# Kernel tuning notes

Measured on AMD Instinct MI355X. Metric: run time of the kernel, lower is better.

The kernel has to match this reference:

```python
import jax, jax.numpy as jnp
import numpy as np

EPS = 1e-6
SIGMA = 0.1  # temperature for pseudo-LBS blend weights


def _quat_rotate(q, v):
    # q: [..., 4] (w, x, y, z) unit quaternions, v: [..., 3]
    qw, qv = q[..., :1], q[..., 1:]
    t = 2.0 * jnp.cross(qv, v)
    return v + qw * t + jnp.cross(qv, t)


def _pairwise_sqdist(a, b):
    # a: [n, d], b: [m, d] -> [n, m]
    return (jnp.sum(a * a, -1, keepdims=True)
            + jnp.sum(b * b, -1)[None, :]
            - 2.0 * (a @ b.T))


def setup_inputs() -> dict:
    N, K, F, V, J, P, M, H = 300000, 80, 64, 6890, 24, 64, 64, 128
    key = jax.random.key(0)
    ks = jax.random.split(key, 16)
    s = lambda i, shape: jax.random.normal(ks[i], shape, dtype=jnp.float32) * 0.05
    return {
        "xyz": jax.random.normal(ks[0], (N, 3), dtype=jnp.float32),
        "feature": jax.random.normal(ks[1], (N, F), dtype=jnp.float32),
        "centers": jax.random.normal(ks[2], (K, F), dtype=jnp.float32),
        "smpl_verts": jax.random.normal(ks[3], (V, 3), dtype=jnp.float32),
        "skinning_weights": jax.random.uniform(ks[4], (V, J), dtype=jnp.float32),
        "body_pose_feature": jax.random.normal(ks[5], (J, P), dtype=jnp.float32),
        "w_body": s(6, (P + F, M)),
        "b_body": jnp.zeros((M,), jnp.float32),
        "w_pos1": s(7, (3 + M, H)),
        "b_pos1": jnp.zeros((H,), jnp.float32),
        "w_pos2": s(8, (H, M)),
        "b_pos2": jnp.zeros((M,), jnp.float32),
        "w_rot": s(9, (M, 4)),
        "b_rot": jnp.zeros((4,), jnp.float32),
        "w_trans": s(10, (M, 3)),
        "b_trans": jnp.zeros((3,), jnp.float32),
    }


def reference(xyz, feature, centers, smpl_verts, skinning_weights,
              body_pose_feature, w_body, b_body, w_pos1, b_pos1,
              w_pos2, b_pos2, w_rot, b_rot, w_trans, b_trans):
    # ---- soft k-means: soft assignment of N points to K garment joints ----
    a = jax.nn.softmax(-_pairwise_sqdist(feature, centers), axis=-1)  # [N, K]
    cnt = a.sum(axis=0) + EPS                                          # [K]
    # weighted segment-reduce: c_assign^T @ xyz, diag(1/count) normalize
    joint_xyz = (a.T @ xyz) / cnt[:, None]      # [K, 3]
    joint_feat = (a.T @ feature) / cnt[:, None]  # [K, F] (cluster centers)

    # ---- KNN (k=1) skin-weight lookup against SMPL canonical verts ----
    idx = jnp.argmin(_pairwise_sqdist(joint_xyz, smpl_verts), axis=-1)  # [K]
    pts_W = skinning_weights[idx]                                        # [K, J]

    # ---- garment pose decoder ----
    body_feat = pts_W @ body_pose_feature                 # [K, P]
    g = jnp.concatenate([body_feat, joint_feat], axis=-1)  # [K, P+F]
    g = jax.nn.gelu(g @ w_body + b_body)                   # [K, M]
    lo, hi = smpl_verts.min(0), smpl_verts.max(0)
    xn = 2.0 * (joint_xyz - lo) / (hi - lo + EPS) - 1.0    # aabb sym-normalize
    h = jax.nn.relu(jnp.concatenate([xn, g], -1) @ w_pos1 + b_pos1)
    g2 = h @ w_pos2 + b_pos2                               # [K, M]
    q = g2 @ w_rot + b_rot
    q = q / (jnp.linalg.norm(q, axis=-1, keepdims=True) + EPS)  # [K, 4]
    t = g2 @ w_trans + b_trans                                   # [K, 3]

    # ---- pseudo-LBS: blend per-joint transforms back to N points ----
    w = jax.nn.softmax(-_pairwise_sqdist(xyz, joint_xyz) / SIGMA, axis=-1)  # [N, K]
    qb = w @ q
    qb = qb / (jnp.linalg.norm(qb, axis=-1, keepdims=True) + EPS)  # [N, 4]
    deformed_xyz = _quat_rotate(qb, xyz) + w @ t                    # [N, 3]
    return deformed_xyz
```

## Files before the change

### kernel.cpp

```cpp
#include <hip/hip_runtime.h>
#include <math.h>

#define N_PTS 300000
#define NJ 80
#define FDIM 64
#define VN 6890
#define NROUND 4688
#define GRID_A 256
#define TOTW 1024
#define SLOT_B 17408

typedef __attribute__((ext_vector_type(8))) short short8;
typedef __attribute__((ext_vector_type(4))) float f32x4;

union Frag { uint32_t u[4]; short8 v; };

__device__ __forceinline__ uint32_t packhi(float a, float b) {
  return (__float_as_uint(a) >> 16) | (__float_as_uint(b) & 0xFFFF0000u);
}
__device__ __forceinline__ uint32_t packlo(float a, float b) {
  float la = a - __uint_as_float(__float_as_uint(a) & 0xFFFF0000u);
  float lb = b - __uint_as_float(__float_as_uint(b) & 0xFFFF0000u);
  return packhi(la, lb);
}

#define DPPF(x, ctrl) __uint_as_float((uint32_t)__builtin_amdgcn_update_dpp( \
    0, (int)__float_as_uint(x), (ctrl), 0xF, 0xF, true))

__device__ __forceinline__ void gl16(const float* g, const void* l) {
  __builtin_amdgcn_global_load_lds(
      (const __attribute__((address_space(1))) void*)g,
      (__attribute__((address_space(3))) void*)l, 16, 0, 0);
}
__device__ __forceinline__ void gl4(const float* g, const void* l) {
  __builtin_amdgcn_global_load_lds(
      (const __attribute__((address_space(1))) void*)g,
      (__attribute__((address_space(3))) void*)l, 4, 0, 0);
}

__global__ __launch_bounds__(256, 1) void kA(
    const float* __restrict__ xyz, const float* __restrict__ feature,
    const float* __restrict__ centers, float* __restrict__ jacc,
    float* __restrict__ part)
{
  __shared__ __align__(16) unsigned char ring[4][2][SLOT_B];
  __shared__ ushort sChi[NJ][72];
  __shared__ ushort sClo[NJ][72];

  const int tid = threadIdx.x;
  const int w = tid >> 6;
  const int l = tid & 63;
  const int i = l & 15;
  const int g = l >> 4;
  const int gw = blockIdx.x * 4 + w;

  auto STAGE = [&](int st, int rs) {
    const float* fb = feature + (size_t)rs * 4096;
    unsigned char* base = &ring[w][st][0];
    const int maxp = min(63, N_PTS - 1 - rs * 64);
#pragma unroll
    for (int k = 0; k < 16; ++k) {
      const int lu = k * 64 + l;
      int ptl = lu >> 4;
      ptl = ptl <= maxp ? ptl : maxp;
      const int gu = ptl * 16 + ((lu & 15) ^ (ptl & 7));
      gl16(fb + gu * 4, base + k * 1024);
    }
    const float* xb = xyz + (size_t)rs * 192;
    const int maxf = 3 * maxp + 2;
#pragma unroll
    for (int k = 0; k < 3; ++k) {
      int fi = k * 64 + l;
      fi = fi <= maxf ? fi : maxf;
      gl4(xb + fi, base + 16384 + k * 256);
    }
  };

  STAGE(0, gw);

  for (int idx = tid; idx < NJ * FDIM; idx += 256) {
    float f = centers[idx];
    sChi[idx >> 6][idx & 63] = (ushort)(__float_as_uint(f) >> 16);
    float lo = f - __uint_as_float(__float_as_uint(f) & 0xFFFF0000u);
    sClo[idx >> 6][idx & 63] = (ushort)(__float_as_uint(lo) >> 16);
  }
  float cn[5];
#pragma unroll
  for (int nt = 0; nt < 5; ++nt) {
    float s = 0.f;
    const float* cp = centers + (size_t)(i + 16 * nt) * FDIM + 8 * g;
#pragma unroll
    for (int e = 0; e < 8; ++e) {
      float a0 = cp[e], a1 = cp[32 + e];
      s += a0 * a0 + a1 * a1;
    }
    s += __shfl_xor(s, 16);
    s += __shfl_xor(s, 32);
    cn[nt] = s;
  }
  __syncthreads();

  f32x4 acc2[5][5];
#pragma unroll
  for (int a = 0; a < 5; ++a)
#pragma unroll
    for (int b = 0; b < 5; ++b) acc2[a][b] = (f32x4){0.f, 0.f, 0.f, 0.f};

  int s2 = 0;
  for (int r = gw; r < NROUND; r += TOTW) {
    {
      int rn = r + TOTW; if (rn > NROUND - 1) rn = NROUND - 1;
      STAGE(s2 ^ 1, rn);
    }
    asm volatile("s_waitcnt vmcnt(19)" ::: "memory");
    __builtin_amdgcn_sched_barrier(0);

    const float* F = (const float*)&ring[w][s2][0];
    const float* X = (const float*)&ring[w][s2][16384];
    const int pbase = r * 64;

    Frag pA[2][5];
#pragma unroll
    for (int cp = 0; cp < 2; ++cp) {
      f32x4 acc1[2][5];
#pragma unroll
      for (int cc = 0; cc < 2; ++cc)
#pragma unroll
        for (int nt = 0; nt < 5; ++nt) acc1[cc][nt] = (f32x4){0.f, 0.f, 0.f, 0.f};

#pragma unroll
      for (int ks = 0; ks < 2; ++ks) {
        Frag ah[2], al[2];
#pragma unroll
        for (int cc = 0; cc < 2; ++cc) {
          const int ptl = 32 * cp + 16 * cc + i;
          const int m = ptl & 7;
          const int j = 8 * ks + 2 * g;
          float4 va = *(const float4*)(F + ptl * 64 + ((j ^ m) << 2));
          float4 vb = *(const float4*)(F + ptl * 64 + (((j + 1) ^ m) << 2));
          ah[cc].u[0] = packhi(va.x, va.y); ah[cc].u[1] = packhi(va.z, va.w);
          ah[cc].u[2] = packhi(vb.x, vb.y); ah[cc].u[3] = packhi(vb.z, vb.w);
          al[cc].u[0] = packlo(va.x, va.y); al[cc].u[1] = packlo(va.z, va.w);
          al[cc].u[2] = packlo(vb.x, vb.y); al[cc].u[3] = packlo(vb.z, vb.w);
        }
#pragma unroll
        for (int nt = 0; nt < 5; ++nt) {
          Frag bh, bl;
          *(uint4*)bh.u = *(const uint4*)&sChi[i + 16 * nt][32 * ks + 8 * g];
          *(uint4*)bl.u = *(const uint4*)&sClo[i + 16 * nt][32 * ks + 8 * g];
#pragma unroll
          for (int cc = 0; cc < 2; ++cc) {
            acc1[cc][nt] = __builtin_amdgcn_mfma_f32_16x16x32_bf16(ah[cc].v, bh.v, acc1[cc][nt], 0, 0, 0);
            acc1[cc][nt] = __builtin_amdgcn_mfma_f32_16x16x32_bf16(al[cc].v, bh.v, acc1[cc][nt], 0, 0, 0);
            acc1[cc][nt] = __builtin_amdgcn_mfma_f32_16x16x32_bf16(ah[cc].v, bl.v, acc1[cc][nt], 0, 0, 0);
          }
        }
      }

#pragma unroll
      for (int cc = 0; cc < 2; ++cc) {
        f32x4 e5[5];
#pragma unroll
        for (int nt = 0; nt < 5; ++nt)
#pragma unroll
          for (int rr = 0; rr < 4; ++rr) e5[nt][rr] = 2.f * acc1[cc][nt][rr] - cn[nt];
        float rs[4];
#pragma unroll
        for (int rr = 0; rr < 4; ++rr) {
          float mm = e5[0][rr];
#pragma unroll
          for (int nt = 1; nt < 5; ++nt) mm = fmaxf(mm, e5[nt][rr]);
          mm = fmaxf(mm, DPPF(mm, 0xB1));
          mm = fmaxf(mm, DPPF(mm, 0x4E));
          mm = fmaxf(mm, DPPF(mm, 0x141));
          mm = fmaxf(mm, DPPF(mm, 0x140));
          float ss = 0.f;
#pragma unroll
          for (int nt = 0; nt < 5; ++nt) {
            float e = __expf(e5[nt][rr] - mm);
            e5[nt][rr] = e;
            ss += e;
          }
          ss += DPPF(ss, 0xB1);
          ss += DPPF(ss, 0x4E);
          ss += DPPF(ss, 0x141);
          ss += DPPF(ss, 0x140);
          rs[rr] = __builtin_amdgcn_rcpf(ss);
        }
        const int pt0 = pbase + 32 * cp + 16 * cc + 4 * g;
#pragma unroll
        for (int nt = 0; nt < 5; ++nt) {
          float p0 = (pt0 + 0 < N_PTS) ? e5[nt][0] * rs[0] : 0.f;
          float p1 = (pt0 + 1 < N_PTS) ? e5[nt][1] * rs[1] : 0.f;
          float p2 = (pt0 + 2 < N_PTS) ? e5[nt][2] * rs[2] : 0.f;
          float p3 = (pt0 + 3 < N_PTS) ? e5[nt][3] * rs[3] : 0.f;
          pA[cp][nt].u[2 * cc + 0] = packhi(p0, p1);
          pA[cp][nt].u[2 * cc + 1] = packhi(p2, p3);
        }
      }
    }

#pragma unroll
    for (int ct = 0; ct < 5; ++ct) {
#pragma unroll
      for (int hf = 0; hf < 2; ++hf) {
        Frag B;
        float x[8];
        if (ct < 4) {
          const int d = 16 * ct + i, jd = d >> 2, db = d & 3;
#pragma unroll
          for (int n = 0; n < 8; ++n) {
            const int pb = (n < 4) ? (4 * g + n) : (16 + 4 * g + (n - 4));
            const int ptl = 32 * hf + pb;
            x[n] = F[ptl * 64 + ((jd ^ (ptl & 7)) << 2) + db];
          }
        } else {
#pragma unroll
          for (int n = 0; n < 8; ++n) {
            const int pb = (n < 4) ? (4 * g + n) : (16 + 4 * g + (n - 4));
            const int ptl = 32 * hf + pb;
            x[n] = (i < 3) ? X[ptl * 3 + i] : (i == 3 ? 1.f : 0.f);
          }
        }
        B.u[0] = packhi(x[0], x[1]); B.u[1] = packhi(x[2], x[3]);
        B.u[2] = packhi(x[4], x[5]); B.u[3] = packhi(x[6], x[7]);
#pragma unroll
        for (int nt = 0; nt < 5; ++nt)
          acc2[nt][ct] = __builtin_amdgcn_mfma_f32_16x16x32_bf16(pA[hf][nt].v, B.v, acc2[nt][ct], 0, 0, 0);
      }
    }

    s2 ^= 1;
  }

  asm volatile("s_waitcnt vmcnt(0)" ::: "memory");
  __syncthreads();
  float* sJ = (float*)&ring[0][0][0];
  for (int idx = tid; idx < 5440; idx += 256) sJ[idx] = 0.f;
  __syncthreads();
#pragma unroll
  for (int ww = 0; ww < 4; ++ww) {
    if (w == ww) {
#pragma unroll
      for (int nt = 0; nt < 5; ++nt)
#pragma unroll
        for (int ct = 0; ct < 5; ++ct) {
          if (ct < 4 || i < 4) {
            const int col = 16 * ct + i;
#pragma unroll
            for (int rr = 0; rr < 4; ++rr)
              sJ[(16 * nt + 4 * g + rr) * 68 + col] += acc2[nt][ct][rr];
          }
        }
    }
    __syncthreads();
  }
  if (part) {
    for (int idx = tid; idx < 5440; idx += 256)
      part[(size_t)blockIdx.x * 5440 + idx] = sJ[idx];
  } else {
    for (int idx = tid; idx < 5440; idx += 256)
      atomicAdd(&jacc[idx], sJ[idx]);
  }
}

__global__ __launch_bounds__(256) void kB(
    const float* __restrict__ jacc, const float* __restrict__ part,
    const float* __restrict__ smpl,
    const float* __restrict__ sw, const float* __restrict__ bpf,
    const float* __restrict__ w_body, const float* __restrict__ b_body,
    const float* __restrict__ w_pos1, const float* __restrict__ b_pos1,
    const float* __restrict__ w_pos2, const float* __restrict__ b_pos2,
    const float* __restrict__ w_rot,  const float* __restrict__ b_rot,
    const float* __restrict__ w_trans,const float* __restrict__ b_trans,
    float* __restrict__ jpack, float* __restrict__ qpack,
    float* __restrict__ tpack)
{
  const int k = blockIdx.x;
  const int tid = threadIdx.x;
  __shared__ float red[3][68];
  __shared__ float sh68[68];
  __shared__ float gin[128];
  __shared__ float in2[67];
  __shared__ float h2[128];
  __shared__ float g2[64];
  __shared__ float q7[8];

  if (part) {
    if (tid < 204) {
      const int c = tid % 68, bg = tid / 68;
      const int b0 = bg * 85, b1 = (bg == 2) ? GRID_A : b0 + 85;
      const float* pk = part + k * 68 + c;
      float s = 0.f;
#pragma unroll 4
      for (int b = b0; b < b1; ++b) s += pk[(size_t)b * 5440];
      red[bg][c] = s;
    }
    __syncthreads();
    if (tid < 68) sh68[tid] = red[0][tid] + red[1][tid] + red[2][tid];
  } else {
    if (tid < 68) sh68[tid] = jacc[k * 68 + tid];
  }
  __syncthreads();

  const float cnt = sh68[67] + 1e-6f;
  const float jx = sh68[64] / cnt;
  const float jy = sh68[65] / cnt;
  const float jz = sh68[66] / cnt;

  if (tid < 64) {
    const int l = tid;
    gin[64 + l] = sh68[l] / cnt;

    float lo0 = 1e30f, lo1 = 1e30f, lo2 = 1e30f;
    float hi0 = -1e30f, hi1 = -1e30f, hi2 = -1e30f;
    float best = 1e30f; int bi = 0;
    for (int v = l; v < VN; v += 64) {
      float x = smpl[v*3], y = smpl[v*3+1], z = smpl[v*3+2];
      lo0 = fminf(lo0, x); hi0 = fmaxf(hi0, x);
      lo1 = fminf(lo1, y); hi1 = fmaxf(hi1, y);
      lo2 = fminf(lo2, z); hi2 = fmaxf(hi2, z);
      float dx = x - jx, dy = y - jy, dz = z - jz;
      float d = dx*dx + dy*dy + dz*dz;
      if (d < best) { best = d; bi = v; }
    }
#pragma unroll
    for (int m = 1; m < 64; m <<= 1) {
      lo0 = fminf(lo0, __shfl_xor(lo0, m));
      lo1 = fminf(lo1, __shfl_xor(lo1, m));
      lo2 = fminf(lo2, __shfl_xor(lo2, m));
      hi0 = fmaxf(hi0, __shfl_xor(hi0, m));
      hi1 = fmaxf(hi1, __shfl_xor(hi1, m));
      hi2 = fmaxf(hi2, __shfl_xor(hi2, m));
      float d2 = __shfl_xor(best, m); int i2 = __shfl_xor(bi, m);
      if (d2 < best || (d2 == best && i2 < bi)) { best = d2; bi = i2; }
    }

    {
      float s = 0.f;
      for (int j = 0; j < 24; ++j) s += sw[bi*24 + j] * bpf[j*64 + l];
      gin[l] = s;
    }
    if (l < 3) {
      float lo = (l == 0) ? lo0 : (l == 1) ? lo1 : lo2;
      float hi = (l == 0) ? hi0 : (l == 1) ? hi1 : hi2;
      float jc = (l == 0) ? jx : (l == 1) ? jy : jz;
      in2[l] = 2.f * (jc - lo) / (hi - lo + 1e-6f) - 1.f;
    }
  }
  __syncthreads();

  if (tid < 64) {
    const int l = tid;
    float s = b_body[l];
    for (int t = 0; t < 128; ++t) s += gin[t] * w_body[t*64 + l];
    float u = 0.7978845608028654f * (s + 0.044715f * s * s * s);
    float e = __expf(2.f * u);
    float th = 1.f - 2.f / (e + 1.f);
    in2[3 + l] = 0.5f * s * (1.f + th);
  }
  __syncthreads();

  if (tid < 64) {
    const int l = tid;
#pragma unroll
    for (int half = 0; half < 2; ++half) {
      const int m = l + 64*half;
      float s = b_pos1[m];
      for (int t = 0; t < 67; ++t) s += in2[t] * w_pos1[t*128 + m];
      h2[m] = fmaxf(s, 0.f);
    }
  }
  __syncthreads();

  if (tid < 64) {
    const int l = tid;
    float s = b_pos2[l];
    for (int t = 0; t < 128; ++t) s += h2[t] * w_pos2[t*64 + l];
    g2[l] = s;
  }
  __syncthreads();

  if (tid < 4) {
    float s = b_rot[tid];
    for (int t = 0; t < 64; ++t) s += g2[t] * w_rot[t*4 + tid];
    q7[tid] = s;
  } else if (tid < 7) {
    const int j = tid - 4;
    float s = b_trans[j];
    for (int t = 0; t < 64; ++t) s += g2[t] * w_trans[t*3 + j];
    q7[tid] = s;
  }
  __syncthreads();
  if (tid == 0) {
    float q0 = q7[0], q1 = q7[1], q2 = q7[2], q3 = q7[3];
    float rn = 1.f / (sqrtf(q0*q0 + q1*q1 + q2*q2 + q3*q3) + 1e-6f);
    *(float4*)&qpack[k*4] = make_float4(q0*rn, q1*rn, q2*rn, q3*rn);
    *(float4*)&tpack[k*4] = make_float4(q7[4], q7[5], q7[6], 0.f);
    *(float4*)&jpack[k*4] = make_float4(jx, jy, jz, jx*jx + jy*jy + jz*jz);
  }
}

__global__ __launch_bounds__(256) void kC(
    const float* __restrict__ xyz, const float* __restrict__ jpack,
    const float* __restrict__ qpack, const float* __restrict__ tpack,
    float* __restrict__ out)
{
  __shared__ float4 sj[NJ], sq[NJ], st[NJ];
  __shared__ float sxy[768];
  const int tid = threadIdx.x;
  const int pbase = blockIdx.x * 256;
  const int nval = min(256, N_PTS - pbase);
  const int cnt3 = nval * 3;

  if (tid < 80)        sj[tid]       = ((const float4*)jpack)[tid];
  else if (tid < 160)  sq[tid - 80]  = ((const float4*)qpack)[tid - 80];
  else if (tid < 240)  st[tid - 160] = ((const float4*)tpack)[tid - 160];
  for (int t = tid; t < cnt3; t += 256) sxy[t] = xyz[(size_t)pbase * 3 + t];
  __syncthreads();

  const bool valid = tid < nval;
  float x0 = 0.f, x1 = 0.f, x2 = 0.f;
  if (valid) { x0 = sxy[tid*3]; x1 = sxy[tid*3+1]; x2 = sxy[tid*3+2]; }
  __syncthreads();

  float lv[NJ];
  float m = -1e30f;
#pragma unroll
  for (int k = 0; k < NJ; ++k) {
    float4 j = sj[k];
    lv[k] = (2.f*(x0*j.x + x1*j.y + x2*j.z) - j.w) * 10.0f;
    m = fmaxf(m, lv[k]);
  }
  float s = 0.f;
  float qb0=0,qb1=0,qb2=0,qb3=0, tb0=0,tb1=0,tb2=0;
#pragma unroll
  for (int k = 0; k < NJ; ++k) {
    float e = __expf(lv[k] - m);
    s += e;
    float4 q = sq[k];
    float4 t = st[k];
    qb0 += e*q.x; qb1 += e*q.y; qb2 += e*q.z; qb3 += e*q.w;
    tb0 += e*t.x; tb1 += e*t.y; tb2 += e*t.z;
  }
  float rs = 1.f / s;
  qb0*=rs; qb1*=rs; qb2*=rs; qb3*=rs; tb0*=rs; tb1*=rs; tb2*=rs;
  float nrm = sqrtf(qb0*qb0+qb1*qb1+qb2*qb2+qb3*qb3) + 1e-6f;
  float rn = 1.f / nrm;
  float qw = qb0*rn, qx = qb1*rn, qy = qb2*rn, qz = qb3*rn;
  float t2x = 2.f*(qy*x2 - qz*x1);
  float t2y = 2.f*(qz*x0 - qx*x2);
  float t2z = 2.f*(qx*x1 - qy*x0);
  float cx = qy*t2z - qz*t2y;
  float cy = qz*t2x - qx*t2z;
  float cz = qx*t2y - qy*t2x;
  float r0 = x0 + qw*t2x + cx + tb0;
  float r1 = x1 + qw*t2y + cy + tb1;
  float r2 = x2 + qw*t2z + cz + tb2;

  if (valid) { sxy[tid*3] = r0; sxy[tid*3+1] = r1; sxy[tid*3+2] = r2; }
  __syncthreads();
  for (int t = tid; t < cnt3; t += 256) out[(size_t)pbase * 3 + t] = sxy[t];
}

extern "C" void kernel_launch(void* const* d_in, const int* in_sizes, int n_in,
                              void* d_out, int out_size, void* d_ws, size_t ws_size,
                              hipStream_t stream) {
  const float* xyz     = (const float*)d_in[0];
  const float* feature = (const float*)d_in[1];
  const float* centers = (const float*)d_in[2];
  const float* smpl    = (const float*)d_in[3];
  const float* sw      = (const float*)d_in[4];
  const float* bpf     = (const float*)d_in[5];
  const float* w_body  = (const float*)d_in[6];
  const float* b_body  = (const float*)d_in[7];
  const float* w_pos1  = (const float*)d_in[8];
  const float* b_pos1  = (const float*)d_in[9];
  const float* w_pos2  = (const float*)d_in[10];
  const float* b_pos2  = (const float*)d_in[11];
  const float* w_rot   = (const float*)d_in[12];
  const float* b_rot   = (const float*)d_in[13];
  const float* w_trans = (const float*)d_in[14];
  const float* b_trans = (const float*)d_in[15];
  float* out = (float*)d_out;

  float* ws    = (float*)d_ws;
  float* jacc  = ws;
  float* jpack = ws + 5440;
  float* qpack = ws + 5760;
  float* tpack = ws + 6080;
  float* part  = ws + 6400;

  const size_t need = (size_t)6400 + (size_t)GRID_A * 5440;
  const bool use_part = (ws_size / 4) >= need;
  float* part_arg = use_part ? part : nullptr;

  if (!use_part) hipMemsetAsync(jacc, 0, 5440 * sizeof(float), stream);
  kA<<<dim3(GRID_A), dim3(256), 0, stream>>>(xyz, feature, centers, jacc, part_arg);
  kB<<<dim3(NJ), dim3(256), 0, stream>>>(jacc, part_arg, smpl, sw, bpf,
                                         w_body, b_body, w_pos1, b_pos1,
                                         w_pos2, b_pos2, w_rot, b_rot,
                                         w_trans, b_trans, jpack, qpack, tpack);
  kC<<<dim3((N_PTS + 255) / 256), dim3(256), 0, stream>>>(xyz, jpack, qpack, tpack, out);
}
```

Measured before the change: 137.1 us.

## Pre-pack features into MFMA B-operand tiles and halve per-round tile size

Adds a pre-pass kernel that converts feature and xyz into bf16 tiles already in the MFMA B-operand layout, so the main kernel's second GEMM loads B fragments directly instead of gathering and packing scalars from LDS. Each round now covers 32 points instead of 64, which shrinks the LDS ring and register footprint. It also folds log2(e) into the centers so the softmax can use exp2 without a per-element multiply. In exchange it adds an extra kernel launch and roughly 48 MB of extra global traffic for the packed copy, and it depends on the workspace being large enough.

```diff
diff --git a/kernel.cpp b/kernel.cpp
--- a/kernel.cpp
+++ b/kernel.cpp
@@ -5,10 +5,11 @@
 #define NJ 80
 #define FDIM 64
 #define VN 6890
-#define NROUND 4688
+#define NROUND 9375
 #define GRID_A 256
 #define TOTW 1024
-#define SLOT_B 17408
+#define SLOT_B 13312
+#define NTILE 9375
 
 typedef __attribute__((ext_vector_type(8))) short short8;
 typedef __attribute__((ext_vector_type(4))) float f32x4;
@@ -23,6 +24,10 @@
   float lb = b - __uint_as_float(__float_as_uint(b) & 0xFFFF0000u);
   return packhi(la, lb);
 }
+__device__ __forceinline__ uint32_t rne16(float f) {
+  uint32_t u = __float_as_uint(f);
+  return (u + 0x7FFFu + ((u >> 16) & 1u)) >> 16;
+}
 
 #define DPPF(x, ctrl) __uint_as_float((uint32_t)__builtin_amdgcn_update_dpp( \
     0, (int)__float_as_uint(x), (ctrl), 0xF, 0xF, true))
@@ -38,10 +43,67 @@
       (__attribute__((address_space(3))) void*)l, 4, 0, 0);
 }
 
+__global__ __launch_bounds__(256) void kF(
+    const float* __restrict__ xyz, const float* __restrict__ feature,
+    unsigned char* __restrict__ dtb)
+{
+  __shared__ float sF[64][68];
+  __shared__ float sx[192];
+  const int tid = threadIdx.x;
+  const int pbase = blockIdx.x * 64;
+  const int t0 = blockIdx.x * 2;
+
+#pragma unroll
+  for (int q = 0; q < 4; ++q) {
+    int idx = tid + 256 * q;
+    int pt = idx >> 4;
+    int dc = (idx & 15) << 2;
+    int gpt = pbase + pt; if (gpt >= N_PTS) gpt = N_PTS - 1;
+    float4 v = *(const float4*)(feature + (size_t)gpt * FDIM + dc);
+    *(float4*)&sF[pt][dc] = v;
+  }
+  if (tid < 192) {
+    int fi = pbase * 3 + tid;
+    if (fi >= N_PTS * 3) fi = N_PTS * 3 - 1;
+    sx[tid] = xyz[fi];
+  }
+  __syncthreads();
+
+  for (int u = tid; u < 640; u += 256) {
+    const int tile2 = u / 320;
+    const int unit  = u % 320;
+    const int gtile = t0 + tile2;
+    if (gtile >= NTILE) continue;
+    const int d  = unit >> 2;
+    const int gp = unit & 3;
+    const int g  = gp ^ ((d >> 2) & 3);
+    uint32_t wk[4];
+#pragma unroll
+    for (int h = 0; h < 4; ++h) {
+      float v0 = 0.f, v1 = 0.f;
+#pragma unroll
+      for (int z = 0; z < 2; ++z) {
+        const int e = 2 * h + z;
+        const int pl = (e < 4) ? (4 * g + e) : (16 + 4 * g + (e - 4));
+        const int p = 32 * tile2 + pl;
+        float v;
+        if (d < 64)       v = sF[p][d];
+        else if (d < 67)  v = sx[p * 3 + (d - 64)];
+        else if (d == 67) v = 1.f;
+        else              v = 0.f;
+        if (z == 0) v0 = v; else v1 = v;
+      }
+      wk[h] = rne16(v0) | (rne16(v1) << 16);
+    }
+    *(uint4*)(dtb + (size_t)gtile * 5120 + (size_t)unit * 16) = *(uint4*)wk;
+  }
+}
+
+template<int MODE>
 __global__ __launch_bounds__(256, 1) void kA(
     const float* __restrict__ xyz, const float* __restrict__ feature,
-    const float* __restrict__ centers, float* __restrict__ jacc,
-    float* __restrict__ part)
+    const float* __restrict__ centers, const unsigned char* __restrict__ dtb,
+    float* __restrict__ jacc, float* __restrict__ part)
 {
   __shared__ __align__(16) unsigned char ring[4][2][SLOT_B];
   __shared__ ushort sChi[NJ][72];
@@ -55,33 +117,38 @@
   const int gw = blockIdx.x * 4 + w;
 
   auto STAGE = [&](int st, int rs) {
-    const float* fb = feature + (size_t)rs * 4096;
+    const float* fb = feature + (size_t)rs * 2048;
     unsigned char* base = &ring[w][st][0];
-    const int maxp = min(63, N_PTS - 1 - rs * 64);
-#pragma unroll
-    for (int k = 0; k < 16; ++k) {
+#pragma unroll
+    for (int k = 0; k < 8; ++k) {
       const int lu = k * 64 + l;
-      int ptl = lu >> 4;
-      ptl = ptl <= maxp ? ptl : maxp;
+      const int ptl = lu >> 4;
       const int gu = ptl * 16 + ((lu & 15) ^ (ptl & 7));
       gl16(fb + gu * 4, base + k * 1024);
     }
-    const float* xb = xyz + (size_t)rs * 192;
-    const int maxf = 3 * maxp + 2;
-#pragma unroll
-    for (int k = 0; k < 3; ++k) {
-      int fi = k * 64 + l;
-      fi = fi <= maxf ? fi : maxf;
-      gl4(xb + fi, base + 16384 + k * 256);
+    if (MODE == 1) {
+      const unsigned char* db = dtb + (size_t)rs * 5120;
+#pragma unroll
+      for (int k = 0; k < 5; ++k)
+        gl16((const float*)(db + (size_t)k * 1024 + (size_t)l * 16),
+             base + 8192 + k * 1024);
+    } else {
+      const float* xb = xyz + (size_t)rs * 96;
+#pragma unroll
+      for (int k = 0; k < 2; ++k) {
+        int fi = k * 64 + l; if (fi > 95) fi = 95;
+        gl4(xb + fi, base + 8192 + k * 256);
+      }
     }
   };
 
   STAGE(0, gw);
 
   for (int idx = tid; idx < NJ * FDIM; idx += 256) {
-    float f = centers[idx];
-    sChi[idx >> 6][idx & 63] = (ushort)(__float_as_uint(f) >> 16);
-    float lo = f - __uint_as_float(__float_as_uint(f) & 0xFFFF0000u);
+    float cp = centers[idx] * 2.8853900817779268f;
+    uint32_t u = __float_as_uint(cp);
+    sChi[idx >> 6][idx & 63] = (ushort)(u >> 16);
+    float lo = cp - __uint_as_float(u & 0xFFFF0000u);
     sClo[idx >> 6][idx & 63] = (ushort)(__float_as_uint(lo) >> 16);
   }
   float cn[5];
@@ -96,7 +163,7 @@
     }
     s += __shfl_xor(s, 16);
     s += __shfl_xor(s, 32);
-    cn[nt] = s;
+    cn[nt] = s * 1.4426950408889634f;
   }
   __syncthreads();
 
@@ -112,122 +179,116 @@
       int rn = r + TOTW; if (rn > NROUND - 1) rn = NROUND - 1;
       STAGE(s2 ^ 1, rn);
     }
-    asm volatile("s_waitcnt vmcnt(19)" ::: "memory");
+    if constexpr (MODE == 1) asm volatile("s_waitcnt vmcnt(13)" ::: "memory");
+    else                     asm volatile("s_waitcnt vmcnt(10)" ::: "memory");
     __builtin_amdgcn_sched_barrier(0);
 
     const float* F = (const float*)&ring[w][s2][0];
-    const float* X = (const float*)&ring[w][s2][16384];
-    const int pbase = r * 64;
-
-    Frag pA[2][5];
-#pragma unroll
-    for (int cp = 0; cp < 2; ++cp) {
-      f32x4 acc1[2][5];
-#pragma unroll
-      for (int cc = 0; cc < 2; ++cc)
-#pragma unroll
-        for (int nt = 0; nt < 5; ++nt) acc1[cc][nt] = (f32x4){0.f, 0.f, 0.f, 0.f};
-
-#pragma unroll
-      for (int ks = 0; ks < 2; ++ks) {
-        Frag ah[2], al[2];
-#pragma unroll
-        for (int cc = 0; cc < 2; ++cc) {
-          const int ptl = 32 * cp + 16 * cc + i;
-          const int m = ptl & 7;
-          const int j = 8 * ks + 2 * g;
-          float4 va = *(const float4*)(F + ptl * 64 + ((j ^ m) << 2));
-          float4 vb = *(const float4*)(F + ptl * 64 + (((j + 1) ^ m) << 2));
-          ah[cc].u[0] = packhi(va.x, va.y); ah[cc].u[1] = packhi(va.z, va.w);
-          ah[cc].u[2] = packhi(vb.x, vb.y); ah[cc].u[3] = packhi(vb.z, vb.w);
-          al[cc].u[0] = packlo(va.x, va.y); al[cc].u[1] = packlo(va.z, va.w);
-          al[cc].u[2] = packlo(vb.x, vb.y); al[cc].u[3] = packlo(vb.z, vb.w);
+    const unsigned char* Fd = &ring[w][s2][8192];
+    const float* X = (const float*)&ring[w][s2][8192];
+
+    f32x4 acc1[2][5];
+#pragma unroll
+    for (int c = 0; c < 2; ++c)
+#pragma unroll
+      for (int nt = 0; nt < 5; ++nt) acc1[c][nt] = (f32x4){0.f, 0.f, 0.f, 0.f};
+
+#pragma unroll
+    for (int ks = 0; ks < 2; ++ks) {
+      Frag ah[2], al[2];
+#pragma unroll
+      for (int c = 0; c < 2; ++c) {
+        const int ptl = 16 * c + i;
+        const int m = ptl & 7;
+        const int j = 8 * ks + 2 * g;
+        float4 va = *(const float4*)(F + ptl * 64 + ((j ^ m) << 2));
+        float4 vb = *(const float4*)(F + ptl * 64 + (((j + 1) ^ m) << 2));
+        ah[c].u[0] = packhi(va.x, va.y); ah[c].u[1] = packhi(va.z, va.w);
+        ah[c].u[2] = packhi(vb.x, vb.y); ah[c].u[3] = packhi(vb.z, vb.w);
+        al[c].u[0] = packlo(va.x, va.y); al[c].u[1] = packlo(va.z, va.w);
+        al[c].u[2] = packlo(vb.x, vb.y); al[c].u[3] = packlo(vb.z, vb.w);
+      }
+#pragma unroll
+      for (int nt = 0; nt < 5; ++nt) {
+        Frag bh, bl;
+        *(uint4*)bh.u = *(const uint4*)&sChi[i + 16 * nt][32 * ks + 8 * g];
+        *(uint4*)bl.u = *(const uint4*)&sClo[i + 16 * nt][32 * ks + 8 * g];
+#pragma unroll
+        for (int c = 0; c < 2; ++c) {
+          acc1[c][nt] = __builtin_amdgcn_mfma_f32_16x16x32_bf16(ah[c].v, bh.v, acc1[c][nt], 0, 0, 0);
+          acc1[c][nt] = __builtin_amdgcn_mfma_f32_16x16x32_bf16(al[c].v, bh.v, acc1[c][nt], 0, 0, 0);
+          acc1[c][nt] = __builtin_amdgcn_mfma_f32_16x16x32_bf16(ah[c].v, bl.v, acc1[c][nt], 0, 0, 0);
         }
+      }
+    }
+
+    Frag pA[5];
+#pragma unroll
+    for (int c = 0; c < 2; ++c) {
+      f32x4 e5[5];
+#pragma unroll
+      for (int nt = 0; nt < 5; ++nt)
+#pragma unroll
+        for (int rr = 0; rr < 4; ++rr) e5[nt][rr] = acc1[c][nt][rr] - cn[nt];
+      float rs[4];
+#pragma unroll
+      for (int rr = 0; rr < 4; ++rr) {
+        float mm = e5[0][rr];
+#pragma unroll
+        for (int nt = 1; nt < 5; ++nt) mm = fmaxf(mm, e5[nt][rr]);
+        mm = fmaxf(mm, DPPF(mm, 0xB1));
+        mm = fmaxf(mm, DPPF(mm, 0x4E));
+        mm = fmaxf(mm, DPPF(mm, 0x141));
+        mm = fmaxf(mm, DPPF(mm, 0x140));
+        float ss = 0.f;
 #pragma unroll
         for (int nt = 0; nt < 5; ++nt) {
-          Frag bh, bl;
-          *(uint4*)bh.u = *(const uint4*)&sChi[i + 16 * nt][32 * ks + 8 * g];
-          *(uint4*)bl.u = *(const uint4*)&sClo[i + 16 * nt][32 * ks + 8 * g];
-#pragma unroll
-          for (int cc = 0; cc < 2; ++cc) {
-            acc1[cc][nt] = __builtin_amdgcn_mfma_f32_16x16x32_bf16(ah[cc].v, bh.v, acc1[cc][nt], 0, 0, 0);
-            acc1[cc][nt] = __builtin_amdgcn_mfma_f32_16x16x32_bf16(al[cc].v, bh.v, acc1[cc][nt], 0, 0, 0);
-            acc1[cc][nt] = __builtin_amdgcn_mfma_f32_16x16x32_bf16(ah[cc].v, bl.v, acc1[cc][nt], 0, 0, 0);
-          }
+          float e = exp2f(e5[nt][rr] - mm);
+          e5[nt][rr] = e;
+          ss += e;
         }
-      }
-
-#pragma unroll
-      for (int cc = 0; cc < 2; ++cc) {
-        f32x4 e5[5];
-#pragma unroll
-        for (int nt = 0; nt < 5; ++nt)
-#pragma unroll
-          for (int rr = 0; rr < 4; ++rr) e5[nt][rr] = 2.f * acc1[cc][nt][rr] - cn[nt];
-        float rs[4];
-#pragma unroll
-        for (int rr = 0; rr < 4; ++rr) {
-          float mm = e5[0][rr];
-#pragma unroll
-          for (int nt = 1; nt < 5; ++nt) mm = fmaxf(mm, e5[nt][rr]);
-          mm = fmaxf(mm, DPPF(mm, 0xB1));
-          mm = fmaxf(mm, DPPF(mm, 0x4E));
-          mm = fmaxf(mm, DPPF(mm, 0x141));
-          mm = fmaxf(mm, DPPF(mm, 0x140));
-          float ss = 0.f;
-#pragma unroll
-          for (int nt = 0; nt < 5; ++nt) {
-            float e = __expf(e5[nt][rr] - mm);
-            e5[nt][rr] = e;
-            ss += e;
-          }
-          ss += DPPF(ss, 0xB1);
-          ss += DPPF(ss, 0x4E);
-          ss += DPPF(ss, 0x141);
-          ss += DPPF(ss, 0x140);
-          rs[rr] = __builtin_amdgcn_rcpf(ss);
-        }
-        const int pt0 = pbase + 32 * cp + 16 * cc + 4 * g;
-#pragma unroll
-        for (int nt = 0; nt < 5; ++nt) {
-          float p0 = (pt0 + 0 < N_PTS) ? e5[nt][0] * rs[0] : 0.f;
-          float p1 = (pt0 + 1 < N_PTS) ? e5[nt][1] * rs[1] : 0.f;
-          float p2 = (pt0 + 2 < N_PTS) ? e5[nt][2] * rs[2] : 0.f;
-          float p3 = (pt0 + 3 < N_PTS) ? e5[nt][3] * rs[3] : 0.f;
-          pA[cp][nt].u[2 * cc + 0] = packhi(p0, p1);
-          pA[cp][nt].u[2 * cc + 1] = packhi(p2, p3);
-        }
+        ss += DPPF(ss, 0xB1);
+        ss += DPPF(ss, 0x4E);
+        ss += DPPF(ss, 0x141);
+        ss += DPPF(ss, 0x140);
+        rs[rr] = __builtin_amdgcn_rcpf(ss);
+      }
+#pragma unroll
+      for (int nt = 0; nt < 5; ++nt) {
+        pA[nt].u[2 * c + 0] = packhi(e5[nt][0] * rs[0], e5[nt][1] * rs[1]);
+        pA[nt].u[2 * c + 1] = packhi(e5[nt][2] * rs[2], e5[nt][3] * rs[3]);
       }
     }
 
 #pragma unroll
     for (int ct = 0; ct < 5; ++ct) {
-#pragma unroll
-      for (int hf = 0; hf < 2; ++hf) {
-        Frag B;
+      Frag B;
+      if constexpr (MODE == 1) {
+        const int d = 16 * ct + i;
+        const int unit = d * 4 + (g ^ ((i >> 2) & 3));
+        *(uint4*)B.u = *(const uint4*)(Fd + unit * 16);
+      } else {
         float x[8];
         if (ct < 4) {
           const int d = 16 * ct + i, jd = d >> 2, db = d & 3;
 #pragma unroll
           for (int n = 0; n < 8; ++n) {
-            const int pb = (n < 4) ? (4 * g + n) : (16 + 4 * g + (n - 4));
-            const int ptl = 32 * hf + pb;
+            const int ptl = (n < 4) ? (4 * g + n) : (16 + 4 * g + (n - 4));
             x[n] = F[ptl * 64 + ((jd ^ (ptl & 7)) << 2) + db];
           }
         } else {
 #pragma unroll
           for (int n = 0; n < 8; ++n) {
-            const int pb = (n < 4) ? (4 * g + n) : (16 + 4 * g + (n - 4));
-            const int ptl = 32 * hf + pb;
+            const int ptl = (n < 4) ? (4 * g + n) : (16 + 4 * g + (n - 4));
             x[n] = (i < 3) ? X[ptl * 3 + i] : (i == 3 ? 1.f : 0.f);
           }
         }
         B.u[0] = packhi(x[0], x[1]); B.u[1] = packhi(x[2], x[3]);
         B.u[2] = packhi(x[4], x[5]); B.u[3] = packhi(x[6], x[7]);
-#pragma unroll
-        for (int nt = 0; nt < 5; ++nt)
-          acc2[nt][ct] = __builtin_amdgcn_mfma_f32_16x16x32_bf16(pA[hf][nt].v, B.v, acc2[nt][ct], 0, 0, 0);
-      }
+      }
+#pragma unroll
+      for (int nt = 0; nt < 5; ++nt)
+        acc2[nt][ct] = __builtin_amdgcn_mfma_f32_16x16x32_bf16(pA[nt].v, B.v, acc2[nt][ct], 0, 0, 0);
     }
 
     s2 ^= 1;
@@ -490,16 +551,31 @@
   float* qpack = ws + 5760;
   float* tpack = ws + 6080;
   float* part  = ws + 6400;
-
-  const size_t need = (size_t)6400 + (size_t)GRID_A * 5440;
-  const bool use_part = (ws_size / 4) >= need;
-  float* part_arg = use_part ? part : nullptr;
-
-  if (!use_part) hipMemsetAsync(jacc, 0, 5440 * sizeof(float), stream);
-  kA<<<dim3(GRID_A), dim3(256), 0, stream>>>(xyz, feature, centers, jacc, part_arg);
-  kB<<<dim3(NJ), dim3(256), 0, stream>>>(jacc, part_arg, smpl, sw, bpf,
-                                         w_body, b_body, w_pos1, b_pos1,
-                                         w_pos2, b_pos2, w_rot, b_rot,
-                                         w_trans, b_trans, jpack, qpack, tpack);
+  const size_t need0 = (size_t)6400 + (size_t)GRID_A * 5440;
+  unsigned char* dtb = (unsigned char*)(ws + need0);
+  const size_t need1 = need0 + (size_t)NTILE * 5120 / 4;
+  const size_t wsf = ws_size / 4;
+
+  if (wsf >= need1) {
+    kF<<<dim3((NTILE + 1) / 2), dim3(256), 0, stream>>>(xyz, feature, dtb);
+    kA<1><<<dim3(GRID_A), dim3(256), 0, stream>>>(xyz, feature, centers, dtb, jacc, part);
+    kB<<<dim3(NJ), dim3(256), 0, stream>>>(jacc, part, smpl, sw, bpf,
+                                           w_body, b_body, w_pos1, b_pos1,
+                                           w_pos2, b_pos2, w_rot, b_rot,
+                                           w_trans, b_trans, jpack, qpack, tpack);
+  } else if (wsf >= need0) {
+    kA<0><<<dim3(GRID_A), dim3(256), 0, stream>>>(xyz, feature, centers, nullptr, jacc, part);
+    kB<<<dim3(NJ), dim3(256), 0, stream>>>(jacc, part, smpl, sw, bpf,
+                                           w_body, b_body, w_pos1, b_pos1,
+                                           w_pos2, b_pos2, w_rot, b_rot,
+                                           w_trans, b_trans, jpack, qpack, tpack);
+  } else {
+    hipMemsetAsync(jacc, 0, 5440 * sizeof(float), stream);
+    kA<0><<<dim3(GRID_A), dim3(256), 0, stream>>>(xyz, feature, centers, nullptr, jacc, nullptr);
+    kB<<<dim3(NJ), dim3(256), 0, stream>>>(jacc, nullptr, smpl, sw, bpf,
+                                           w_body, b_body, w_pos1, b_pos1,
+                                           w_pos2, b_pos2, w_rot, b_rot,
+                                           w_trans, b_trans, jpack, qpack, tpack);
+  }
   kC<<<dim3((N_PTS + 255) / 256), dim3(256), 0, stream>>>(xyz, jpack, qpack, tpack, out);
 }
```

After: 161.5 us. 17.8% more time.
